# Kernel optimization log

Hardware: AMD Instinct MI355X
Metric: run time of the kernel (lower is better)

## Reference

```python
import jax, jax.numpy as jnp
import numpy as np

N_NODES = 50000
N_EDGES = 600000
N_GRAPHS = 64
D = 128  # node/edge/global feature dim
NUM_CLASSES = 10
NUM_PASSES = 3


def setup_inputs() -> dict:
    key = jax.random.key(0)
    ks = jax.random.split(key, 12)
    node_attr = jax.random.normal(ks[0], (N_NODES, D), jnp.float32)
    edge_attr = jax.random.normal(ks[1], (N_EDGES, D), jnp.float32)
    u = jax.random.normal(ks[2], (N_GRAPHS, D), jnp.float32)
    edge_index = jax.random.randint(ks[3], (2, N_EDGES), 0, N_NODES, jnp.int64 if jax.config.jax_enable_x64 else jnp.int32)
    batch = jnp.sort(jax.random.randint(ks[4], (N_NODES,), 0, N_GRAPHS, jnp.int32))
    s = 1.0 / np.sqrt(D)
    We_w = jax.random.normal(ks[5], (4 * D, D), jnp.float32) * s
    We_b = jnp.zeros((D,), jnp.float32)
    Wn_w = jax.random.normal(ks[6], (3 * D, D), jnp.float32) * s
    Wn_b = jnp.zeros((D,), jnp.float32)
    Wg_w = jax.random.normal(ks[7], (3 * D, D), jnp.float32) * s
    Wg_b = jnp.zeros((D,), jnp.float32)
    lin_w = jax.random.normal(ks[8], (3 * D, NUM_CLASSES), jnp.float32) * s
    lin_b = jnp.zeros((NUM_CLASSES,), jnp.float32)
    return {"node_attr": node_attr, "edge_attr": edge_attr, "u": u,
            "edge_index": edge_index, "batch": batch,
            "We_w": We_w, "We_b": We_b, "Wn_w": Wn_w, "Wn_b": Wn_b,
            "Wg_w": Wg_w, "Wg_b": Wg_b, "lin_w": lin_w, "lin_b": lin_b}


def _segment_mean(x, seg, num_segments):
    s = jax.ops.segment_sum(x, seg, num_segments=num_segments)
    cnt = jax.ops.segment_sum(jnp.ones((x.shape[0],), x.dtype), seg, num_segments=num_segments)
    return s / jnp.maximum(cnt, 1.0)[:, None]


def reference(node_attr, edge_attr, u, edge_index, batch,
              We_w, We_b, Wn_w, Wn_b, Wg_w, Wg_b, lin_w, lin_b):
    src = edge_index[0]
    dst = edge_index[1]
    n_nodes = node_attr.shape[0]
    n_graphs = u.shape[0]
    edge_bar = None
    for _ in range(NUM_PASSES):
        # edge update: phi_e([h_src, h_dst, e, u[batch_src]])
        e_in = jnp.concatenate(
            [node_attr[src], node_attr[dst], edge_attr, u[batch[src]]], axis=1)
        edge_attr = jax.nn.relu(e_in @ We_w + We_b)
        # node update: mean of incoming edges per dest node, then phi_n
        edge_bar = _segment_mean(edge_attr, dst, n_nodes)  # [N, D]
        n_in = jnp.concatenate([node_attr, edge_bar, u[batch]], axis=1)
        node_attr = jax.nn.relu(n_in @ Wn_w + Wn_b)
        # global update: per-graph means, then phi_g
        node_mean = _segment_mean(node_attr, batch, n_graphs)
        eb_mean = _segment_mean(edge_bar, batch, n_graphs)
        g_in = jnp.concatenate([node_mean, eb_mean, u], axis=1)
        u = jax.nn.relu(g_in @ Wg_w + Wg_b)
    # readout: concat + global mean pool + linear classifier
    graph_attr = jnp.concatenate([node_attr, edge_bar, u[batch]], axis=1)  # [N, 3D]
    pooled = _segment_mean(graph_attr, batch, n_graphs)  # [G, 3D]
    return pooled @ lin_w + lin_b
```

## Files before the change

kernel.cpp:

```cpp
#include <hip/hip_runtime.h>
#include <math.h>

#define D 128

typedef short bf16x8 __attribute__((ext_vector_type(8)));
typedef float f32x4 __attribute__((ext_vector_type(4)));

__device__ __forceinline__ ushort f2b(float f) {
    union { float f; unsigned u; } v; v.f = f;
    unsigned r = v.u + 0x7FFFu + ((v.u >> 16) & 1u);
    return (ushort)(r >> 16);
}
__device__ __forceinline__ float b2f(ushort b) {
    union { unsigned u; float f; } v; v.u = ((unsigned)b) << 16;
    return v.f;
}
__device__ __forceinline__ void gl_lds16(const void* g, void* l) {
    __builtin_amdgcn_global_load_lds(
        (const __attribute__((address_space(1))) void*)g,
        (__attribute__((address_space(3))) void*)l, 16, 0, 0);
}
__device__ __forceinline__ int lower_bound_i(const int* __restrict__ a, int n, int v) {
    int lo = 0, hi = n;
    while (lo < hi) { int m = (lo + hi) >> 1; if (a[m] < v) lo = m + 1; else hi = m; }
    return lo;
}

__global__ void count_kernel(const int* __restrict__ dst, int* __restrict__ cnt, int E) {
    int e = blockIdx.x * blockDim.x + threadIdx.x;
    if (e < E) atomicAdd(&cnt[dst[e]], 1);
}

__global__ void scan_kernel(const int* __restrict__ cnt, int* __restrict__ offs, int N) {
    __shared__ int part[1024];
    const int t = threadIdx.x;
    const int chunk = (N + 1023) >> 10;
    int lo = t * chunk; if (lo > N) lo = N;
    int hi = lo + chunk; if (hi > N) hi = N;
    int s = 0;
    for (int i = lo; i < hi; ++i) s += cnt[i];
    part[t] = s;
    __syncthreads();
    if (t == 0) {
        int a = 0;
        for (int i = 0; i < 1024; ++i) { int v = part[i]; part[i] = a; a += v; }
        offs[N] = a;
    }
    __syncthreads();
    int a = part[t];
    for (int i = lo; i < hi; ++i) { offs[i] = a; a += cnt[i]; }
}

__global__ void scatter_kernel(const int* __restrict__ dst, const int* __restrict__ offs,
                               int* __restrict__ fill, int* __restrict__ csr, int E) {
    int e = blockIdx.x * blockDim.x + threadIdx.x;
    if (e < E) {
        int d = dst[e];
        int p = offs[d] + atomicAdd(&fill[d], 1);
        csr[p] = e;
    }
}

__global__ void prep_kernel(
    float* __restrict__ edge,
    const float* __restrict__ node, ushort* __restrict__ node_bf,
    const float* __restrict__ u, ushort* __restrict__ u_bf,
    const float* __restrict__ We_w, ushort* __restrict__ Bt12, ushort* __restrict__ W3t,
    const float* __restrict__ Wn_w, ushort* __restrict__ Wnt,
    int N, int G, int E)
{
    const int gid = blockIdx.x * 256 + threadIdx.x;
    const int c0 = E * 32;
    const int c1 = c0 + N * D / 4;
    const int c2 = c1 + G * D / 4;
    const int c3 = c2 + 512 * D;
    const int c4 = c3 + 384 * D;
    if (gid < c0) {
        int row = gid >> 5, q = gid & 31;
        float4 v = *(const float4*)(edge + (size_t)row * D + q * 4);
        ushort4 o; o.x = f2b(v.x); o.y = f2b(v.y); o.z = f2b(v.z); o.w = f2b(v.w);
        *(ushort4*)((ushort*)edge + (size_t)row * 256 + q * 4) = o;
    } else if (gid < c1) {
        int i = (gid - c0) * 4;
        float4 v = *(const float4*)(node + i);
        ushort4 o; o.x = f2b(v.x); o.y = f2b(v.y); o.z = f2b(v.z); o.w = f2b(v.w);
        *(ushort4*)(node_bf + i) = o;
    } else if (gid < c2) {
        int i = (gid - c1) * 4;
        float4 v = *(const float4*)(u + i);
        ushort4 o; o.x = f2b(v.x); o.y = f2b(v.y); o.z = f2b(v.z); o.w = f2b(v.w);
        *(ushort4*)(u_bf + i) = o;
    } else if (gid < c3) {
        int i = gid - c2;
        int k = i >> 7, n = i & 127;
        if (k < 384) {
            ushort b = f2b(We_w[i]);
            if (k < 256)
                Bt12[(((size_t)((k >> 7) << 7) + n) << 7) + (k & 127)] = b;
            else
                W3t[((size_t)n << 7) + (k - 256)] = b;
        }
    } else if (gid < c4) {
        int i = gid - c3;
        int k = i >> 7, n = i & 127;
        Wnt[(size_t)n * 384 + k] = f2b(Wn_w[i]);
    }
}

__global__ void uproj_kernel(const float* __restrict__ u, const float* __restrict__ We_w,
                             const float* __restrict__ We_b, float* __restrict__ upf)
{
    __shared__ float us[128];
    const int g = blockIdx.x;
    const int j = threadIdx.x;
    us[j] = u[g * D + j];
    __syncthreads();
    float s = We_b[j];
    for (int k = 0; k < 128; ++k) s += us[k] * We_w[(size_t)(384 + k) * D + j];
    upf[g * D + j] = s;
}

__global__ __launch_bounds__(256) void nproj_gemm(
    const ushort* __restrict__ node_bf, const ushort* __restrict__ Bt12,
    float* __restrict__ npf, int N)
{
    __shared__ ushort As[128 * 32];
    __shared__ ushort Bs[256 * 32];

    const int tid = threadIdx.x;
    const int w = tid >> 6, l = tid & 63;
    const int n0 = blockIdx.x * 128;

    f32x4 acc[4][8];
#pragma unroll
    for (int i = 0; i < 4; ++i)
#pragma unroll
        for (int j = 0; j < 8; ++j) acc[i][j] = (f32x4)0.0f;

    const int wm = (w >> 1) * 64, wn = (w & 1) * 128;
    const int srow = l >> 2;
    const int part = (l & 3) * 8;

    for (int c = 0; c < 4; ++c) {
        const int kl = c * 32;
#pragma unroll
        for (int t = 0; t < 2; ++t) {
            const int s = w + t * 4;
            int n = n0 + s * 16 + srow; if (n >= N) n = N - 1;
            gl_lds16(node_bf + (size_t)n * D + kl + part, &As[s * 512]);
        }
#pragma unroll
        for (int t = 0; t < 4; ++t) {
            const int s = w * 4 + t;
            const int n = s * 16 + srow;
            gl_lds16(Bt12 + (size_t)n * 128 + kl + part, &Bs[s * 512]);
        }
        __syncthreads();

        bf16x8 af[4], bfr[8];
#pragma unroll
        for (int i = 0; i < 4; ++i)
            af[i] = *(const bf16x8*)&As[(wm + i * 16 + (l & 15)) * 32 + (l >> 4) * 8];
#pragma unroll
        for (int j = 0; j < 8; ++j)
            bfr[j] = *(const bf16x8*)&Bs[(wn + j * 16 + (l & 15)) * 32 + (l >> 4) * 8];
#pragma unroll
        for (int i = 0; i < 4; ++i)
#pragma unroll
            for (int j = 0; j < 8; ++j)
                acc[i][j] = __builtin_amdgcn_mfma_f32_16x16x32_bf16(af[i], bfr[j], acc[i][j], 0, 0, 0);
        __syncthreads();
    }

#pragma unroll
    for (int i = 0; i < 4; ++i) {
#pragma unroll
        for (int r = 0; r < 4; ++r) {
            const int m = wm + i * 16 + (l >> 4) * 4 + r;
            const int n = n0 + m;
            if (n < N) {
#pragma unroll
                for (int j = 0; j < 8; ++j)
                    npf[(size_t)n * 256 + wn + j * 16 + (l & 15)] = acc[i][j][r];
            }
        }
    }
}

__global__ __launch_bounds__(256, 2) void edge_gemm(
    ushort* __restrict__ edge_u,
    const float* __restrict__ npf, const float* __restrict__ upf,
    const int* __restrict__ src, const int* __restrict__ dst,
    const int* __restrict__ batch,
    const ushort* __restrict__ W3t, int E)
{
    __shared__ ushort As[256 * 32];
    __shared__ ushort Bs[128 * 32];
    __shared__ int rs[256], rd[256], rb[256];

    const int tid = threadIdx.x;
    const int w = tid >> 6, l = tid & 63;
    const int e0 = blockIdx.x * 256;

    {
        int e = e0 + tid; if (e >= E) e = E - 1;
        int s = src[e];
        rs[tid] = s; rd[tid] = dst[e]; rb[tid] = batch[s];
    }

    f32x4 acc[4][8];
#pragma unroll
    for (int i = 0; i < 4; ++i)
#pragma unroll
        for (int j = 0; j < 8; ++j) acc[i][j] = (f32x4)0.0f;

    const int wm = w * 64;
    const int srow = l >> 2;
    const int part = (l & 3) * 8;

    __syncthreads();

    for (int c = 0; c < 4; ++c) {
        const int kl = c * 32;

#pragma unroll
        for (int t = 0; t < 4; ++t) {
            const int s = w * 4 + t;
            int e = e0 + s * 16 + srow; if (e >= E) e = E - 1;
            gl_lds16(edge_u + (size_t)e * 256 + kl + part, &As[s * 512]);
        }
#pragma unroll
        for (int t = 0; t < 2; ++t) {
            const int s = w + t * 4;
            const int n = s * 16 + srow;
            gl_lds16(W3t + (size_t)n * 128 + kl + part, &Bs[s * 512]);
        }
        __syncthreads();

        bf16x8 af[4], bfr[8];
#pragma unroll
        for (int i = 0; i < 4; ++i)
            af[i] = *(const bf16x8*)&As[(wm + i * 16 + (l & 15)) * 32 + (l >> 4) * 8];
#pragma unroll
        for (int j = 0; j < 8; ++j)
            bfr[j] = *(const bf16x8*)&Bs[(j * 16 + (l & 15)) * 32 + (l >> 4) * 8];
#pragma unroll
        for (int i = 0; i < 4; ++i)
#pragma unroll
            for (int j = 0; j < 8; ++j)
                acc[i][j] = __builtin_amdgcn_mfma_f32_16x16x32_bf16(af[i], bfr[j], acc[i][j], 0, 0, 0);
        __syncthreads();
    }

    const int cc = l & 15;
#pragma unroll
    for (int i = 0; i < 4; ++i) {
#pragma unroll
        for (int r = 0; r < 4; ++r) {
            const int m = wm + i * 16 + (l >> 4) * 4 + r;
            const int e = e0 + m;
            if (e < E) {
                const float* p1 = npf + (size_t)rs[m] * 256;
                const float* p2 = npf + (size_t)rd[m] * 256 + 128;
                const float* pu = upf + (size_t)rb[m] * D;
                ushort* ep = edge_u + (size_t)e * 256;
#pragma unroll
                for (int j = 0; j < 8; ++j) {
                    const int col = j * 16 + cc;
                    float v = acc[i][j][r] + p1[col] + p2[col] + pu[col];
                    ep[col] = f2b(fmaxf(v, 0.0f));
                }
            }
        }
    }
}

__global__ void gather_ebar(const ushort* __restrict__ edge_u, const int* __restrict__ offs,
                            const int* __restrict__ csr, ushort* __restrict__ ebar_bf, int N)
{
    int n = blockIdx.x * 8 + (threadIdx.x >> 5);
    int q = threadIdx.x & 31;
    if (n >= N) return;
    int lo = offs[n], hi = offs[n + 1];
    float s0 = 0.0f, s1 = 0.0f, s2 = 0.0f, s3 = 0.0f;
    for (int j = lo; j < hi; ++j) {
        int e = csr[j];
        ushort4 v = *(const ushort4*)(edge_u + (size_t)e * 256 + q * 4);
        s0 += b2f(v.x); s1 += b2f(v.y); s2 += b2f(v.z); s3 += b2f(v.w);
    }
    float inv = 1.0f / (float)max(hi - lo, 1);
    ushort4 o; o.x = f2b(s0 * inv); o.y = f2b(s1 * inv); o.z = f2b(s2 * inv); o.w = f2b(s3 * inv);
    *(ushort4*)(ebar_bf + (size_t)n * D + q * 4) = o;
}

__global__ __launch_bounds__(256) void node_gemm(
    ushort* __restrict__ node_bf, const ushort* __restrict__ ebar_bf,
    const ushort* __restrict__ u_bf, const int* __restrict__ batch,
    const ushort* __restrict__ Wt, const float* __restrict__ bias, int N)
{
    __shared__ ushort As[128 * 32];
    __shared__ ushort Bs[128 * 32];
    __shared__ int rb[128];

    const int tid = threadIdx.x;
    const int w = tid >> 6, l = tid & 63;
    const int n0 = blockIdx.x * 128;

    if (tid < 128) {
        int n = n0 + tid; if (n >= N) n = N - 1;
        rb[tid] = batch[n];
    }

    f32x4 acc[4][4];
#pragma unroll
    for (int i = 0; i < 4; ++i)
#pragma unroll
        for (int j = 0; j < 4; ++j) acc[i][j] = (f32x4)0.0f;

    const int wm = (w >> 1) * 64, wn = (w & 1) * 64;
    float bj4[4];
#pragma unroll
    for (int j = 0; j < 4; ++j) bj4[j] = bias[wn + j * 16 + (l & 15)];

    const int srow = l >> 2;
    const int part = (l & 3) * 8;

    __syncthreads();

    for (int c = 0; c < 12; ++c) {
        const int srcsel = c >> 2;
        const int kl = (c & 3) * 32;

#pragma unroll
        for (int t = 0; t < 2; ++t) {
            const int s = w + t * 4;
            const int row = s * 16 + srow;
            int n = n0 + row; if (n >= N) n = N - 1;
            const ushort* gp;
            if (srcsel == 0)      gp = node_bf + (size_t)n * D + kl + part;
            else if (srcsel == 1) gp = ebar_bf + (size_t)n * D + kl + part;
            else                  gp = u_bf + (size_t)rb[row] * D + kl + part;
            gl_lds16(gp, &As[s * 512]);
        }
#pragma unroll
        for (int t = 0; t < 2; ++t) {
            const int s = w + t * 4;
            const int n = s * 16 + srow;
            gl_lds16(Wt + (size_t)n * 384 + c * 32 + part, &Bs[s * 512]);
        }
        __syncthreads();

        bf16x8 af[4], bfr[4];
#pragma unroll
        for (int i = 0; i < 4; ++i)
            af[i] = *(const bf16x8*)&As[(wm + i * 16 + (l & 15)) * 32 + (l >> 4) * 8];
#pragma unroll
        for (int j = 0; j < 4; ++j)
            bfr[j] = *(const bf16x8*)&Bs[(wn + j * 16 + (l & 15)) * 32 + (l >> 4) * 8];
#pragma unroll
        for (int i = 0; i < 4; ++i)
#pragma unroll
            for (int j = 0; j < 4; ++j)
                acc[i][j] = __builtin_amdgcn_mfma_f32_16x16x32_bf16(af[i], bfr[j], acc[i][j], 0, 0, 0);
        __syncthreads();
    }

#pragma unroll
    for (int i = 0; i < 4; ++i) {
#pragma unroll
        for (int r = 0; r < 4; ++r) {
            const int m = wm + i * 16 + (l >> 4) * 4 + r;
            const int n = n0 + m;
            if (n < N) {
#pragma unroll
                for (int j = 0; j < 4; ++j) {
                    float v = fmaxf(acc[i][j][r] + bj4[j], 0.0f);
                    node_bf[(size_t)n * D + wn + j * 16 + (l & 15)] = f2b(v);
                }
            }
        }
    }
}

__global__ void reduce_partial(
    const ushort* __restrict__ node_bf, const ushort* __restrict__ ebar_bf,
    const int* __restrict__ batch,
    float* __restrict__ nsum, float* __restrict__ esum, int N)
{
    const int col = threadIdx.x & 127;
    const int half = threadIdx.x >> 7;
    const int r0 = blockIdx.x * 128;
    float sn = 0.0f, se = 0.0f;
    int cur = -1;
    for (int ri = half; ri < 128; ri += 2) {
        int r = r0 + ri;
        if (r >= N) break;
        int g = batch[r];
        if (g != cur) {
            if (cur >= 0) {
                atomicAdd(&nsum[cur * D + col], sn);
                atomicAdd(&esum[cur * D + col], se);
            }
            cur = g; sn = 0.0f; se = 0.0f;
        }
        sn += b2f(node_bf[(size_t)r * D + col]);
        se += b2f(ebar_bf[(size_t)r * D + col]);
    }
    if (cur >= 0) {
        atomicAdd(&nsum[cur * D + col], sn);
        atomicAdd(&esum[cur * D + col], se);
    }
}

__global__ void finalize_global(
    float* __restrict__ nsum, float* __restrict__ esum,
    const int* __restrict__ batch,
    float* __restrict__ nmean, float* __restrict__ emean,
    float* __restrict__ u, ushort* __restrict__ u_bf,
    const float* __restrict__ W, const float* __restrict__ bias, int N)
{
    __shared__ float gin[384];
    __shared__ int cnt_s;
    const int g = blockIdx.x;
    const int j = threadIdx.x;
    if (j == 0) {
        int lo = lower_bound_i(batch, N, g);
        int hi = lower_bound_i(batch, N, g + 1);
        cnt_s = hi - lo;
    }
    __syncthreads();
    float inv = 1.0f / (float)max(cnt_s, 1);
    float nm = nsum[g * D + j] * inv;
    float em = esum[g * D + j] * inv;
    nmean[g * D + j] = nm;
    emean[g * D + j] = em;
    nsum[g * D + j] = 0.0f;
    esum[g * D + j] = 0.0f;
    gin[j] = nm; gin[128 + j] = em; gin[256 + j] = u[g * D + j];
    __syncthreads();
    float s = bias[j];
    for (int k = 0; k < 384; ++k) s += gin[k] * W[(size_t)k * D + j];
    float v = fmaxf(s, 0.0f);
    u[g * D + j] = v;
    u_bf[g * D + j] = f2b(v);
}

__global__ void out_kernel(
    const float* __restrict__ nmean, const float* __restrict__ emean,
    const float* __restrict__ u, const int* __restrict__ batch,
    const float* __restrict__ lw, const float* __restrict__ lb,
    float* __restrict__ out, int N, int NC)
{
    __shared__ float pin[384];
    __shared__ int cntg;
    const int g = blockIdx.x;
    const int t = threadIdx.x;
    if (t == 0) {
        int lo = lower_bound_i(batch, N, g);
        int hi = lower_bound_i(batch, N, g + 1);
        cntg = hi - lo;
    }
    __syncthreads();
    if (t < 128)       pin[t] = nmean[g * D + t];
    else if (t < 256)  pin[t] = emean[g * D + (t - 128)];
    else               pin[t] = (cntg > 0) ? u[g * D + (t - 256)] : 0.0f;
    __syncthreads();
    int c = t >> 5, wv = t & 31;
    if (c < NC) {
        float s = 0.0f;
        for (int k = wv; k < 384; k += 32) s += pin[k] * lw[(size_t)k * NC + c];
#pragma unroll
        for (int off = 16; off > 0; off >>= 1) s += __shfl_down(s, off, 32);
        if (wv == 0) out[g * NC + c] = s + lb[c];
    }
}

extern "C" void kernel_launch(void* const* d_in, const int* in_sizes, int n_in,
                              void* d_out, int out_size, void* d_ws, size_t ws_size,
                              hipStream_t stream) {
    float* node = (float*)d_in[0];
    float* edge = (float*)d_in[1];
    float* u    = (float*)d_in[2];
    const int* eidx  = (const int*)d_in[3];
    const int* batch = (const int*)d_in[4];
    const float* We_w = (const float*)d_in[5];
    const float* We_b = (const float*)d_in[6];
    const float* Wn_w = (const float*)d_in[7];
    const float* Wn_b = (const float*)d_in[8];
    const float* Wg_w = (const float*)d_in[9];
    const float* Wg_b = (const float*)d_in[10];
    const float* lin_w = (const float*)d_in[11];
    const float* lin_b = (const float*)d_in[12];

    const int N = in_sizes[0] / D;
    const int E = in_sizes[3] / 2;
    const int G = in_sizes[2] / D;
    const int NC = out_size / G;
    const int* src = eidx;
    const int* dst = eidx + E;

    char* p = (char*)d_ws;
    auto carve = [&](size_t bytes) { void* r = p; p += (bytes + 255) & ~(size_t)255; return r; };
    int*    cnt     = (int*)carve((size_t)N * 4);
    int*    fill    = (int*)carve((size_t)N * 4);
    float*  nsum    = (float*)carve((size_t)G * D * 4);
    float*  esum    = (float*)carve((size_t)G * D * 4);
    size_t  zspan   = (size_t)(p - (char*)cnt);
    int*    offs    = (int*)carve((size_t)(N + 1) * 4);
    int*    csr     = (int*)carve((size_t)E * 4);
    ushort* node_bf = (ushort*)carve((size_t)N * D * 2);
    ushort* ebar_bf = (ushort*)carve((size_t)N * D * 2);
    ushort* u_bf    = (ushort*)carve((size_t)G * D * 2);
    ushort* Bt12    = (ushort*)carve((size_t)256 * 128 * 2);
    ushort* W3t     = (ushort*)carve((size_t)128 * 128 * 2);
    ushort* Wnt     = (ushort*)carve((size_t)384 * D * 2);
    float*  nmean   = (float*)carve((size_t)G * D * 4);
    float*  emean   = (float*)carve((size_t)G * D * 4);
    float*  upf     = (float*)carve((size_t)G * D * 4);
    float*  npf     = (float*)carve((size_t)N * 256 * 4);

    ushort* edge_u = (ushort*)edge;

    hipMemsetAsync(cnt, 0, zspan, stream);

    count_kernel<<<(E + 255) / 256, 256, 0, stream>>>(dst, cnt, E);
    scan_kernel<<<1, 1024, 0, stream>>>(cnt, offs, N);
    scatter_kernel<<<(E + 255) / 256, 256, 0, stream>>>(dst, offs, fill, csr, E);

    const int prep_units = E * 32 + N * D / 4 + G * D / 4 + 512 * D + 384 * D;
    prep_kernel<<<(prep_units + 255) / 256, 256, 0, stream>>>(
        edge, node, node_bf, u, u_bf, We_w, Bt12, W3t, Wn_w, Wnt, N, G, E);

    const int edge_blocks = (E + 255) / 256;
    const int node_blocks = (N + 127) / 128;
    const int proj_blocks = (N + 127) / 128;
    const int red_blocks  = (N + 127) / 128;

    for (int pass = 0; pass < 3; ++pass) {
        uproj_kernel<<<G, 128, 0, stream>>>(u, We_w, We_b, upf);
        nproj_gemm<<<proj_blocks, 256, 0, stream>>>(node_bf, Bt12, npf, N);
        edge_gemm<<<edge_blocks, 256, 0, stream>>>(edge_u, npf, upf, src, dst, batch,
                                                   W3t, E);
        gather_ebar<<<(N + 7) / 8, 256, 0, stream>>>(edge_u, offs, csr, ebar_bf, N);
        node_gemm<<<node_blocks, 256, 0, stream>>>(node_bf, ebar_bf, u_bf, batch,
                                                   Wnt, Wn_b, N);
        reduce_partial<<<red_blocks, 256, 0, stream>>>(node_bf, ebar_bf, batch, nsum, esum, N);
        finalize_global<<<G, 128, 0, stream>>>(nsum, esum, batch, nmean, emean,
                                               u, u_bf, Wg_w, Wg_b, N);
    }
    out_kernel<<<G, 384, 0, stream>>>(nmean, emean, u, batch, lin_w, lin_b,
                                      (float*)d_out, N, NC);
}
```

Measured before the change: 1.331 ms.

## Fold u-projection into node projection and vectorize edge epilogue via column permutation

The per-graph u projection is now added once per source node inside the node-projection GEMM epilogue, so the edge GEMM no longer gathers batch[src] and upf for every edge. The B-matrix rows are loaded in a permuted order so each lane owns 8 contiguous output columns. That lets both epilogues use float4 gathers and 16-byte bf16 stores instead of scalar strided accesses. The permutation must line up exactly with the MFMA output layout, which adds a correctness risk.

```diff
diff --git a/kernel.cpp b/kernel.cpp
--- a/kernel.cpp
+++ b/kernel.cpp
@@ -5,6 +5,7 @@
 
 typedef short bf16x8 __attribute__((ext_vector_type(8)));
 typedef float f32x4 __attribute__((ext_vector_type(4)));
+typedef ushort ushort8 __attribute__((ext_vector_type(8)));
 
 __device__ __forceinline__ ushort f2b(float f) {
     union { float f; unsigned u; } v; v.f = f;
@@ -122,14 +123,21 @@
 
 __global__ __launch_bounds__(256) void nproj_gemm(
     const ushort* __restrict__ node_bf, const ushort* __restrict__ Bt12,
+    const float* __restrict__ upf, const int* __restrict__ batch,
     float* __restrict__ npf, int N)
 {
     __shared__ ushort As[128 * 32];
     __shared__ ushort Bs[256 * 32];
+    __shared__ int rbs[128];
 
     const int tid = threadIdx.x;
     const int w = tid >> 6, l = tid & 63;
     const int n0 = blockIdx.x * 128;
+
+    if (tid < 128) {
+        int n = n0 + tid; if (n >= N) n = N - 1;
+        rbs[tid] = batch[n];
+    }
 
     f32x4 acc[4][8];
 #pragma unroll
@@ -152,7 +160,9 @@
 #pragma unroll
         for (int t = 0; t < 4; ++t) {
             const int s = w * 4 + t;
-            const int n = s * 16 + srow;
+            const int br = s * 16 + srow;
+            const int h = br >> 7, b7 = br & 127;
+            const int n = (h << 7) | ((b7 & 15) << 3) | (b7 >> 4);
             gl_lds16(Bt12 + (size_t)n * 128 + kl + part, &Bs[s * 512]);
         }
         __syncthreads();
@@ -172,16 +182,30 @@
         __syncthreads();
     }
 
+    const int cc = l & 15;
+    const int qr = (l >> 4) * 4;
 #pragma unroll
     for (int i = 0; i < 4; ++i) {
 #pragma unroll
         for (int r = 0; r < 4; ++r) {
-            const int m = wm + i * 16 + (l >> 4) * 4 + r;
+            const int m = wm + i * 16 + qr + r;
             const int n = n0 + m;
             if (n < N) {
-#pragma unroll
-                for (int j = 0; j < 8; ++j)
-                    npf[(size_t)n * 256 + wn + j * 16 + (l & 15)] = acc[i][j][r];
+                float4 u0 = make_float4(0.f, 0.f, 0.f, 0.f);
+                float4 u1 = make_float4(0.f, 0.f, 0.f, 0.f);
+                if (wn == 0) {
+                    const float* pu = upf + (size_t)rbs[m] * D + cc * 8;
+                    u0 = *(const float4*)pu;
+                    u1 = *(const float4*)(pu + 4);
+                }
+                float4 o0, o1;
+                o0.x = acc[i][0][r] + u0.x; o0.y = acc[i][1][r] + u0.y;
+                o0.z = acc[i][2][r] + u0.z; o0.w = acc[i][3][r] + u0.w;
+                o1.x = acc[i][4][r] + u1.x; o1.y = acc[i][5][r] + u1.y;
+                o1.z = acc[i][6][r] + u1.z; o1.w = acc[i][7][r] + u1.w;
+                float* op = npf + (size_t)n * 256 + wn + cc * 8;
+                *(float4*)op = o0;
+                *(float4*)(op + 4) = o1;
             }
         }
     }
@@ -189,14 +213,13 @@
 
 __global__ __launch_bounds__(256, 2) void edge_gemm(
     ushort* __restrict__ edge_u,
-    const float* __restrict__ npf, const float* __restrict__ upf,
+    const float* __restrict__ npf,
     const int* __restrict__ src, const int* __restrict__ dst,
-    const int* __restrict__ batch,
     const ushort* __restrict__ W3t, int E)
 {
     __shared__ ushort As[256 * 32];
     __shared__ ushort Bs[128 * 32];
-    __shared__ int rs[256], rd[256], rb[256];
+    __shared__ int rs[256], rd[256];
 
     const int tid = threadIdx.x;
     const int w = tid >> 6, l = tid & 63;
@@ -204,8 +227,7 @@
 
     {
         int e = e0 + tid; if (e >= E) e = E - 1;
-        int s = src[e];
-        rs[tid] = s; rd[tid] = dst[e]; rb[tid] = batch[s];
+        rs[tid] = src[e]; rd[tid] = dst[e];
     }
 
     f32x4 acc[4][8];
@@ -232,7 +254,8 @@
 #pragma unroll
         for (int t = 0; t < 2; ++t) {
             const int s = w + t * 4;
-            const int n = s * 16 + srow;
+            const int br = s * 16 + srow;
+            const int n = ((br & 15) << 3) | (br >> 4);
             gl_lds16(W3t + (size_t)n * 128 + kl + part, &Bs[s * 512]);
         }
         __syncthreads();
@@ -253,23 +276,30 @@
     }
 
     const int cc = l & 15;
+    const int qr = (l >> 4) * 4;
 #pragma unroll
     for (int i = 0; i < 4; ++i) {
 #pragma unroll
         for (int r = 0; r < 4; ++r) {
-            const int m = wm + i * 16 + (l >> 4) * 4 + r;
+            const int m = wm + i * 16 + qr + r;
             const int e = e0 + m;
             if (e < E) {
-                const float* p1 = npf + (size_t)rs[m] * 256;
-                const float* p2 = npf + (size_t)rd[m] * 256 + 128;
-                const float* pu = upf + (size_t)rb[m] * D;
-                ushort* ep = edge_u + (size_t)e * 256;
-#pragma unroll
-                for (int j = 0; j < 8; ++j) {
-                    const int col = j * 16 + cc;
-                    float v = acc[i][j][r] + p1[col] + p2[col] + pu[col];
-                    ep[col] = f2b(fmaxf(v, 0.0f));
-                }
+                const float* p1 = npf + (size_t)rs[m] * 256 + cc * 8;
+                const float* p2 = npf + (size_t)rd[m] * 256 + 128 + cc * 8;
+                float4 a0 = *(const float4*)p1;
+                float4 a1 = *(const float4*)(p1 + 4);
+                float4 b0 = *(const float4*)p2;
+                float4 b1 = *(const float4*)(p2 + 4);
+                ushort8 o;
+                o[0] = f2b(fmaxf(acc[i][0][r] + a0.x + b0.x, 0.0f));
+                o[1] = f2b(fmaxf(acc[i][1][r] + a0.y + b0.y, 0.0f));
+                o[2] = f2b(fmaxf(acc[i][2][r] + a0.z + b0.z, 0.0f));
+                o[3] = f2b(fmaxf(acc[i][3][r] + a0.w + b0.w, 0.0f));
+                o[4] = f2b(fmaxf(acc[i][4][r] + a1.x + b1.x, 0.0f));
+                o[5] = f2b(fmaxf(acc[i][5][r] + a1.y + b1.y, 0.0f));
+                o[6] = f2b(fmaxf(acc[i][6][r] + a1.z + b1.z, 0.0f));
+                o[7] = f2b(fmaxf(acc[i][7][r] + a1.w + b1.w, 0.0f));
+                *(ushort8*)(edge_u + (size_t)e * 256 + cc * 8) = o;
             }
         }
     }
@@ -538,9 +568,8 @@
 
     for (int pass = 0; pass < 3; ++pass) {
         uproj_kernel<<<G, 128, 0, stream>>>(u, We_w, We_b, upf);
-        nproj_gemm<<<proj_blocks, 256, 0, stream>>>(node_bf, Bt12, npf, N);
-        edge_gemm<<<edge_blocks, 256, 0, stream>>>(edge_u, npf, upf, src, dst, batch,
-                                                   W3t, E);
+        nproj_gemm<<<proj_blocks, 256, 0, stream>>>(node_bf, Bt12, upf, batch, npf, N);
+        edge_gemm<<<edge_blocks, 256, 0, stream>>>(edge_u, npf, src, dst, W3t, E);
         gather_ebar<<<(N + 7) / 8, 256, 0, stream>>>(edge_u, offs, csr, ebar_bf, N);
         node_gemm<<<node_blocks, 256, 0, stream>>>(node_bf, ebar_bf, u_bf, batch,
                                                    Wnt, Wn_b, N);
```

After: 1.329 ms. Within noise of the previous version (-0.1%).
